# Performance work log

Hardware: AMD Instinct MI355X
Metric: run time of the kernel (lower is better)

The kernel has to match this reference:

```python
import jax, jax.numpy as jnp
import numpy as np

B, C, T = 16, 256, 2048  # C == embedding_dim D
K, D = 8192, 256
BETA = 0.25


def setup_inputs() -> dict:
    key = jax.random.key(0)
    k1, k2 = jax.random.split(key)
    latents = jax.random.normal(k1, (B, C, T), dtype=jnp.float32)
    # mimic nn.Embedding.weight.data.uniform_(-1/K, 1/K)
    emb_weight = jax.random.uniform(k2, (K, D), dtype=jnp.float32,
                                    minval=-1.0 / K, maxval=1.0 / K)
    return {"latents": latents, "emb_weight": emb_weight}


def reference(latents, emb_weight):
    # [B, C, T] -> [B, T, C]
    lat = jnp.transpose(latents, (0, 2, 1))
    flat = lat.reshape(-1, D)                       # [N, D], N = B*T
    dist = (jnp.sum(flat ** 2, axis=1, keepdims=True)
            + jnp.sum(emb_weight ** 2, axis=1)
            - 2.0 * jnp.matmul(flat, emb_weight.T))
    idx = jnp.argmin(dist, axis=1)                  # [N]
    quantized = emb_weight[idx].reshape(lat.shape)  # [B, T, C]
    e_latent_loss = jnp.mean((jax.lax.stop_gradient(quantized) - lat) ** 2)
    q_latent_loss = jnp.mean((quantized - jax.lax.stop_gradient(lat)) ** 2)
    loss = q_latent_loss + BETA * e_latent_loss
    # straight-through estimator
    quantized = lat + jax.lax.stop_gradient(quantized - lat)
    quantized = jnp.transpose(quantized, (0, 2, 1))  # [B, C, T]
    return quantized, loss, idx.reshape(B, T)
```

## Files before the change

### kernel.cpp

```cpp
#include <hip/hip_runtime.h>

#define B_ 16
#define C_ 256
#define T_ 2048
#define K_ 8192
#define D_ 256
#define N_ (B_ * T_)
#define OUTQ ((size_t)B_ * C_ * T_)

#define BM 128
#define CHUNK 64
#define NCHUNK (K_ / CHUNK)
#define MARGINF 4e-4f
#define BIASF 0.03125f
#define QCAP 1024

typedef __attribute__((ext_vector_type(8))) short bf16x8;
typedef __attribute__((ext_vector_type(4))) float f32x4;

__device__ __forceinline__ unsigned f2bf(float f) {
  unsigned u = __float_as_uint(f);
  return (u + 0x7FFFu + ((u >> 16) & 1u)) >> 16;
}
__device__ __forceinline__ unsigned umin_(unsigned a, unsigned b){return a<b?a:b;}
__device__ __forceinline__ unsigned umax_(unsigned a, unsigned b){return a>b?a:b;}

#define GLDS(g, l) __builtin_amdgcn_global_load_lds( \
    (const __attribute__((address_space(1))) void*)(g), \
    (__attribute__((address_space(3))) void*)(l), 16, 0, 0)

__global__ __launch_bounds__(256) void ebf_prep_kernel(
    const float* __restrict__ emb, unsigned char* __restrict__ ebf)
{
  int gid  = blockIdx.x * 256 + threadIdx.x;
  int code = gid >> 6, dq = gid & 63;
  float4 v = *reinterpret_cast<const float4*>(emb + (size_t)code * D_ + dq * 4);
  unsigned lo = f2bf(v.x) | (f2bf(v.y) << 16);
  unsigned hi = f2bf(v.z) | (f2bf(v.w) << 16);
  unsigned off = code * 512 + ((dq * 8) ^ ((code & 15) << 4));
  *reinterpret_cast<uint2*>(ebf + off) = make_uint2(lo, hi);
}

__global__ __launch_bounds__(256, 1) void vq_argmin_kernel(
    const float* __restrict__ lat, const float* __restrict__ emb,
    const unsigned char* __restrict__ ebf, int* __restrict__ idx_out)
{
  __shared__ __align__(16) unsigned char Ebuf[2][CHUNK * 512];
  __shared__ unsigned rmaxU[2][BM];
  __shared__ unsigned long long bestp[BM];
  __shared__ unsigned qlist[QCAP];
  __shared__ int qn;

  const int tid  = threadIdx.x;
  const int lane = tid & 63;
  const int w    = tid >> 6;
  const int rg   = w >> 1;
  const int cg   = w & 1;
  const int kg   = lane >> 4;
  const int l15  = lane & 15;

  const int n0    = blockIdx.x * BM;
  const int bb    = n0 >> 11;
  const int tbase = n0 & (T_ - 1);
  const float* latb = lat + (size_t)bb * C_ * T_;

  if (tid == 0) qn = 0;
  if (tid < BM) bestp[tid] = ~0ull;

  {
    const unsigned char* src = ebf + w * 8192 + lane * 16;
    unsigned char* dst = &Ebuf[0][w * 8192];
    #pragma unroll
    for (int j = 0; j < 8; ++j) GLDS(src + j * 1024, dst + j * 1024);
  }

  bf16x8 A[4][8];
  #pragma unroll
  for (int rf = 0; rf < 4; ++rf) {
    const int t = tbase + rg * 64 + rf * 16 + l15;
    const float* lp = latb + t;
    #pragma unroll
    for (int ks = 0; ks < 8; ++ks) {
      const int c0 = ks * 32 + kg * 8;
      bf16x8 a;
      #pragma unroll
      for (int j = 0; j < 8; ++j)
        a[j] = (short)f2bf(lp[(size_t)(c0 + j) * T_]);
      A[rf][ks] = a;
    }
  }
  __syncthreads();

  unsigned m1[16], m2[16];
  #pragma unroll
  for (int s = 0; s < 16; ++s) { m1[s] = 0u; m2[s] = 0u; }
  const unsigned kv0 = cg * 32 + l15;

  for (int ch = 0; ch < NCHUNK; ++ch) {
    const int pb = ch & 1;
    if (ch + 1 < NCHUNK) {
      const unsigned char* src =
          ebf + (size_t)(ch + 1) * (CHUNK * 512) + w * 8192 + lane * 16;
      unsigned char* dst = &Ebuf[pb ^ 1][w * 8192];
      #pragma unroll
      for (int j = 0; j < 8; ++j) GLDS(src + j * 1024, dst + j * 1024);
    }

    bf16x8 Bf[2][8];
    const unsigned char* bbase = &Ebuf[pb][0];
    #pragma unroll
    for (int cf = 0; cf < 2; ++cf) {
      const int code_l = cg * 32 + cf * 16 + l15;
      #pragma unroll
      for (int ks = 0; ks < 8; ++ks) {
        const unsigned off = code_l * 512 + ((ks * 64 + kg * 16) ^ (l15 << 4));
        Bf[cf][ks] = *reinterpret_cast<const bf16x8*>(bbase + off);
      }
    }

    #pragma unroll
    for (int cf = 0; cf < 2; ++cf) {
      const unsigned kv = kv0 + (unsigned)(ch * 64 + cf * 16);
      #pragma unroll
      for (int rf = 0; rf < 4; ++rf) {
        f32x4 acc = {BIASF, BIASF, BIASF, BIASF};
        #pragma unroll
        for (int ks = 0; ks < 8; ++ks)
          acc = __builtin_amdgcn_mfma_f32_16x16x32_bf16(A[rf][ks], Bf[cf][ks],
                                                        acc, 0, 0, 0);
        #pragma unroll
        for (int r = 0; r < 4; ++r) {
          const unsigned p = (__float_as_uint(acc[r]) & 0xFFFFE000u) | kv;
          const int s = rf * 4 + r;
          const unsigned mn = umin_(p, m1[s]);
          m1[s] = umax_(p, m1[s]);
          m2[s] = umax_(m2[s], mn);
        }
      }
    }
    __syncthreads();
  }

  #pragma unroll
  for (int s = 0; s < 16; ++s) {
    unsigned v = m1[s];
    v = umax_(v, __shfl_xor(v, 1));
    v = umax_(v, __shfl_xor(v, 2));
    v = umax_(v, __shfl_xor(v, 4));
    v = umax_(v, __shfl_xor(v, 8));
    const int row = rg * 64 + (s >> 2) * 16 + kg * 4 + (s & 3);
    rmaxU[cg][row] = v;
  }
  __syncthreads();

  #pragma unroll
  for (int s = 0; s < 16; ++s) {
    const int row = rg * 64 + (s >> 2) * 16 + kg * 4 + (s & 3);
    const unsigned rm = umax_(rmaxU[0][row], rmaxU[1][row]);
    const float thr = __uint_as_float(rm & 0xFFFFE000u) - MARGINF;
    #pragma unroll
    for (int which = 0; which < 2; ++which) {
      const unsigned m = which ? m2[s] : m1[s];
      if (__uint_as_float(m & 0xFFFFE000u) >= thr) {
        int id = atomicAdd(&qn, 1);
        if (id < QCAP) qlist[id] = ((unsigned)row << 13) | (m & 0x1FFFu);
      }
    }
  }
  __syncthreads();

  const int nq = qn < QCAP ? qn : QCAP;
  for (int i = tid; i < nq; i += 256) {
    const unsigned e = qlist[i];
    const int row = (int)(e >> 13);
    const int k   = (int)(e & 0x1FFFu);
    const int t   = tbase + row;
    const float* xp = latb + t;
    const float* ep = emb + (size_t)k * D_;
    float x2 = 0.f, e2 = 0.f;
    double da = 0.0;
    {
      #pragma clang fp contract(off)
      for (int c = 0; c < D_; ++c) {
        const float xv = xp[(size_t)c * T_];
        const float ev = ep[c];
        const float xs = xv * xv; x2 = x2 + xs;
        const float es = ev * ev; e2 = e2 + es;
        da = fma((double)xv, (double)ev, da);
      }
    }
    float dist;
    {
      #pragma clang fp contract(off)
      const float mmf = (float)da;
      const float tk  = x2 + e2;
      const float two = 2.0f * mmf;
      dist = tk - two;
    }
    const unsigned long long pk =
        ((unsigned long long)__float_as_uint(dist) << 32) | (unsigned)k;
    atomicMin(&bestp[row], pk);
  }
  __syncthreads();
  if (tid < BM) idx_out[n0 + tid] = (int)(bestp[tid] & 0xFFFFFFFFu);
}

__global__ __launch_bounds__(256) void vq_out_kernel(
    const float* __restrict__ lat, const float* __restrict__ emb,
    const int* __restrict__ idx, float* __restrict__ outq,
    double* __restrict__ partial)
{
  __shared__ double sred[256];
  const int gid = blockIdx.x;
  const int b   = gid >> 5;
  const int t0  = (gid & 31) * 64;
  const int tl  = threadIdx.x & 63;
  const int cq  = threadIdx.x >> 6;
  const int t   = t0 + tl;
  const int n   = idx[b * T_ + t];
  const float* ep = emb + (size_t)n * D_;
  double lsum = 0.0;
  for (int ci = 0; ci < 64; ++ci) {
    const int c = cq * 64 + ci;
    const size_t off = ((size_t)b * C_ + c) * T_ + t;
    const float q = ep[c];
    const float l = lat[off];
    outq[off] = q;
    const double d = (double)q - (double)l;
    lsum += d * d;
  }
  sred[threadIdx.x] = lsum;
  __syncthreads();
  for (int s = 128; s > 0; s >>= 1) {
    if (threadIdx.x < s) sred[threadIdx.x] += sred[threadIdx.x + s];
    __syncthreads();
  }
  if (threadIdx.x == 0) partial[gid] = sred[0];
}

__global__ __launch_bounds__(256) void vq_loss_kernel(
    const double* __restrict__ partial, float* __restrict__ out_loss)
{
  __shared__ double sred[256];
  double s = 0.0;
  for (int i = threadIdx.x; i < 512; i += 256) s += partial[i];
  sred[threadIdx.x] = s;
  __syncthreads();
  for (int st = 128; st > 0; st >>= 1) {
    if (threadIdx.x < st) sred[threadIdx.x] += sred[threadIdx.x + st];
    __syncthreads();
  }
  if (threadIdx.x == 0) {
    double m = sred[0] / (double)OUTQ;
    out_loss[0] = (float)(m + 0.25 * m);
  }
}

__global__ __launch_bounds__(256) void vq_idxcopy_kernel(
    const int* __restrict__ idx, float* __restrict__ outi)
{
  int i = blockIdx.x * 256 + threadIdx.x;
  if (i < N_) outi[i] = (float)idx[i];
}

extern "C" void kernel_launch(void* const* d_in, const int* in_sizes, int n_in,
                              void* d_out, int out_size, void* d_ws, size_t ws_size,
                              hipStream_t stream)
{
  const float* lat = (const float*)d_in[0];
  const float* emb = (const float*)d_in[1];

  float* outq     = (float*)d_out;
  float* out_loss = outq + OUTQ;
  float* out_idx  = outq + OUTQ + 1;

  unsigned char* ebf = (unsigned char*)d_out;
  int*    idx     = (int*)d_ws;
  double* partial = (double*)((char*)d_ws + (size_t)N_ * sizeof(int));

  ebf_prep_kernel  <<<2048,     256, 0, stream>>>(emb, ebf);
  vq_argmin_kernel <<<N_ / BM,  256, 0, stream>>>(lat, emb, ebf, idx);
  vq_out_kernel    <<<512,      256, 0, stream>>>(lat, emb, idx, outq, partial);
  vq_loss_kernel   <<<1,        256, 0, stream>>>(partial, out_loss);
  vq_idxcopy_kernel<<<N_ / 256, 256, 0, stream>>>(idx, out_idx);
}
```

Before: 371.9 us.

## Widen argmin blocks to 512 threads, stage gathered codes in LDS, fuse idx cast

```diff
diff --git a/kernel.cpp b/kernel.cpp
--- a/kernel.cpp
+++ b/kernel.cpp
@@ -9,8 +9,9 @@
 #define OUTQ ((size_t)B_ * C_ * T_)
 
 #define BM 128
-#define CHUNK 64
+#define CHUNK 128
 #define NCHUNK (K_ / CHUNK)
+#define NTHR 512
 #define MARGINF 4e-4f
 #define BIASF 0.03125f
 #define QCAP 1024
@@ -41,12 +42,13 @@
   *reinterpret_cast<uint2*>(ebf + off) = make_uint2(lo, hi);
 }
 
-__global__ __launch_bounds__(256, 1) void vq_argmin_kernel(
+__global__ __launch_bounds__(NTHR, 2) void vq_argmin_kernel(
     const float* __restrict__ lat, const float* __restrict__ emb,
-    const unsigned char* __restrict__ ebf, int* __restrict__ idx_out)
+    const unsigned char* __restrict__ ebf, int* __restrict__ idx_out,
+    float* __restrict__ idxf_out)
 {
   __shared__ __align__(16) unsigned char Ebuf[2][CHUNK * 512];
-  __shared__ unsigned rmaxU[2][BM];
+  __shared__ unsigned rmaxU[4][BM];
   __shared__ unsigned long long bestp[BM];
   __shared__ unsigned qlist[QCAP];
   __shared__ int qn;
@@ -54,8 +56,8 @@
   const int tid  = threadIdx.x;
   const int lane = tid & 63;
   const int w    = tid >> 6;
-  const int rg   = w >> 1;
-  const int cg   = w & 1;
+  const int rg   = w >> 2;
+  const int cg   = w & 3;
   const int kg   = lane >> 4;
   const int l15  = lane & 15;
 
@@ -106,27 +108,23 @@
       for (int j = 0; j < 8; ++j) GLDS(src + j * 1024, dst + j * 1024);
     }
 
-    bf16x8 Bf[2][8];
     const unsigned char* bbase = &Ebuf[pb][0];
     #pragma unroll
     for (int cf = 0; cf < 2; ++cf) {
       const int code_l = cg * 32 + cf * 16 + l15;
+      bf16x8 Bf[8];
       #pragma unroll
       for (int ks = 0; ks < 8; ++ks) {
         const unsigned off = code_l * 512 + ((ks * 64 + kg * 16) ^ (l15 << 4));
-        Bf[cf][ks] = *reinterpret_cast<const bf16x8*>(bbase + off);
-      }
-    }
-
-    #pragma unroll
-    for (int cf = 0; cf < 2; ++cf) {
-      const unsigned kv = kv0 + (unsigned)(ch * 64 + cf * 16);
+        Bf[ks] = *reinterpret_cast<const bf16x8*>(bbase + off);
+      }
+      const unsigned kv = kv0 + (unsigned)(ch * CHUNK + cf * 16);
       #pragma unroll
       for (int rf = 0; rf < 4; ++rf) {
         f32x4 acc = {BIASF, BIASF, BIASF, BIASF};
         #pragma unroll
         for (int ks = 0; ks < 8; ++ks)
-          acc = __builtin_amdgcn_mfma_f32_16x16x32_bf16(A[rf][ks], Bf[cf][ks],
+          acc = __builtin_amdgcn_mfma_f32_16x16x32_bf16(A[rf][ks], Bf[ks],
                                                         acc, 0, 0, 0);
         #pragma unroll
         for (int r = 0; r < 4; ++r) {
@@ -156,7 +154,8 @@
   #pragma unroll
   for (int s = 0; s < 16; ++s) {
     const int row = rg * 64 + (s >> 2) * 16 + kg * 4 + (s & 3);
-    const unsigned rm = umax_(rmaxU[0][row], rmaxU[1][row]);
+    const unsigned rm = umax_(umax_(rmaxU[0][row], rmaxU[1][row]),
+                              umax_(rmaxU[2][row], rmaxU[3][row]));
     const float thr = __uint_as_float(rm & 0xFFFFE000u) - MARGINF;
     #pragma unroll
     for (int which = 0; which < 2; ++which) {
@@ -170,7 +169,7 @@
   __syncthreads();
 
   const int nq = qn < QCAP ? qn : QCAP;
-  for (int i = tid; i < nq; i += 256) {
+  for (int i = tid; i < nq; i += NTHR) {
     const unsigned e = qlist[i];
     const int row = (int)(e >> 13);
     const int k   = (int)(e & 0x1FFFu);
@@ -202,7 +201,11 @@
     atomicMin(&bestp[row], pk);
   }
   __syncthreads();
-  if (tid < BM) idx_out[n0 + tid] = (int)(bestp[tid] & 0xFFFFFFFFu);
+  if (tid < BM) {
+    const int k = (int)(bestp[tid] & 0xFFFFFFFFu);
+    idx_out[n0 + tid]  = k;
+    idxf_out[n0 + tid] = (float)k;
+  }
 }
 
 __global__ __launch_bounds__(256) void vq_out_kernel(
@@ -210,20 +213,34 @@
     const int* __restrict__ idx, float* __restrict__ outq,
     double* __restrict__ partial)
 {
+  __shared__ float Ecol[256][65];
   __shared__ double sred[256];
   const int gid = blockIdx.x;
   const int b   = gid >> 5;
   const int t0  = (gid & 31) * 64;
-  const int tl  = threadIdx.x & 63;
-  const int cq  = threadIdx.x >> 6;
-  const int t   = t0 + tl;
-  const int n   = idx[b * T_ + t];
-  const float* ep = emb + (size_t)n * D_;
+
+  {
+    const int r4 = threadIdx.x >> 6, c4 = threadIdx.x & 63;
+    for (int it = 0; it < 16; ++it) {
+      const int r = it * 4 + r4;
+      const int n = idx[b * T_ + t0 + r];
+      const float4 v =
+          *reinterpret_cast<const float4*>(emb + (size_t)n * D_ + c4 * 4);
+      Ecol[c4 * 4 + 0][r] = v.x;
+      Ecol[c4 * 4 + 1][r] = v.y;
+      Ecol[c4 * 4 + 2][r] = v.z;
+      Ecol[c4 * 4 + 3][r] = v.w;
+    }
+  }
+  __syncthreads();
+
+  const int cq = threadIdx.x >> 6, tl = threadIdx.x & 63;
+  const int t  = t0 + tl;
   double lsum = 0.0;
   for (int ci = 0; ci < 64; ++ci) {
     const int c = cq * 64 + ci;
     const size_t off = ((size_t)b * C_ + c) * T_ + t;
-    const float q = ep[c];
+    const float q = Ecol[c][tl];
     const float l = lat[off];
     outq[off] = q;
     const double d = (double)q - (double)l;
@@ -256,13 +273,6 @@
   }
 }
 
-__global__ __launch_bounds__(256) void vq_idxcopy_kernel(
-    const int* __restrict__ idx, float* __restrict__ outi)
-{
-  int i = blockIdx.x * 256 + threadIdx.x;
-  if (i < N_) outi[i] = (float)idx[i];
-}
-
 extern "C" void kernel_launch(void* const* d_in, const int* in_sizes, int n_in,
                               void* d_out, int out_size, void* d_ws, size_t ws_size,
                               hipStream_t stream)
@@ -278,9 +288,8 @@
   int*    idx     = (int*)d_ws;
   double* partial = (double*)((char*)d_ws + (size_t)N_ * sizeof(int));
 
-  ebf_prep_kernel  <<<2048,     256, 0, stream>>>(emb, ebf);
-  vq_argmin_kernel <<<N_ / BM,  256, 0, stream>>>(lat, emb, ebf, idx);
-  vq_out_kernel    <<<512,      256, 0, stream>>>(lat, emb, idx, outq, partial);
-  vq_loss_kernel   <<<1,        256, 0, stream>>>(partial, out_loss);
-  vq_idxcopy_kernel<<<N_ / 256, 256, 0, stream>>>(idx, out_idx);
-}
+  ebf_prep_kernel  <<<2048,    256,  0, stream>>>(emb, ebf);
+  vq_argmin_kernel <<<N_ / BM, NTHR, 0, stream>>>(lat, emb, ebf, idx, out_idx);
+  vq_out_kernel    <<<512,     256,  0, stream>>>(lat, emb, idx, outq, partial);
+  vq_loss_kernel   <<<1,       256,  0, stream>>>(partial, out_loss);
+}
```

New measurement: 318.8 us. -14.3%, faster.
